# Kernel optimization log

Measured on AMD Instinct MI355X. Metric: run time of the kernel, lower is better.

## Reference

```python
import jax, jax.numpy as jnp
import numpy as np

N, D, H_ENC, NZ, K, H_EXP, C = 32768, 1024, 512, 64, 16, 256, 10


def setup_inputs() -> dict:
    key = jax.random.key(0)
    ks = jax.random.split(key, 12)
    s = 0.02
    return {
        "X": jax.random.normal(ks[0], (N, D), dtype=jnp.float32),
        "enc_W": jax.random.normal(ks[1], (D, H_ENC), dtype=jnp.float32) * s,
        "enc_b": jnp.zeros((H_ENC,), dtype=jnp.float32),
        "z_W": jax.random.normal(ks[2], (H_ENC, NZ), dtype=jnp.float32) * s,
        "z_b": jnp.zeros((NZ,), dtype=jnp.float32),
        "mu": jax.random.normal(ks[3], (K, NZ), dtype=jnp.float32),  # cluster_layer
        "W1": jax.random.normal(ks[4], (K, NZ, H_EXP), dtype=jnp.float32) * s,
        "b1": jnp.zeros((K, H_EXP), dtype=jnp.float32),
        "W2": jax.random.normal(ks[5], (K, H_EXP, C), dtype=jnp.float32) * s,
        "b2": jnp.zeros((K, C), dtype=jnp.float32),
    }


def reference(X, enc_W, enc_b, z_W, z_b, mu, W1, b1, W2, b2):
    # AE encoder: Linear-ReLU -> z_layer
    h = jax.nn.relu(X @ enc_W + enc_b)                 # [N, H_ENC]
    z = h @ z_W + z_b                                  # [N, NZ]
    # source_distribution (Student-t, alpha=1; exponent (alpha+1)/2 = 1)
    dist = jnp.sum((z[:, None, :] - mu[None, :, :]) ** 2, axis=-1)  # [N, K]
    q = 1.0 / (1.0 + dist)
    q = q / jnp.sum(q, axis=1, keepdims=True)          # [N, K]
    # per-expert Linear-ReLU-Linear over full batch (attention=True path)
    eh = jax.nn.relu(jnp.einsum("nd,kdh->nkh", z, W1) + b1[None])  # [N, K, H_EXP]
    logits = jnp.einsum("nkh,khc->nkc", eh, W2) + b2[None]         # [N, K, C]
    # soft combine: preds[:, c] += q[:, k] * logits[:, k, c]
    preds = jnp.einsum("nk,nkc->nc", q, logits)        # [N, C]
    return preds
```

## Files before the change

### kernel.cpp

```cpp
#include <hip/hip_runtime.h>
#include <stdint.h>

#define N_ROWS 32768
#define DIM    1024
#define HENC   512
#define NZ     64
#define KE     16
#define HEXP   256
#define NC     10

typedef __attribute__((ext_vector_type(8))) __bf16 bf16x8;
typedef __attribute__((ext_vector_type(4))) float f32x4;
typedef __attribute__((ext_vector_type(8))) unsigned short u16x8;
typedef __attribute__((ext_vector_type(4))) unsigned short u16x4;

__device__ __forceinline__ unsigned short f2bf(float f) {
    __bf16 h = (__bf16)f;
    return __builtin_bit_cast(unsigned short, h);
}

__device__ __forceinline__ void gload_lds16(void* lds, const void* gsrc) {
    __builtin_amdgcn_global_load_lds(
        (const __attribute__((address_space(1))) unsigned int*)gsrc,
        (__attribute__((address_space(3))) unsigned int*)lds,
        16, 0, 0);
}

#define SWZ(col, row) ((col) ^ (((row) & 7) << 3))

__global__ void prep_weights(const float* __restrict__ enc_W,
                             const float* __restrict__ z_W,
                             const float* __restrict__ W1,
                             const float* __restrict__ W2,
                             unsigned short* __restrict__ enc_Wt,
                             unsigned short* __restrict__ z_Wt,
                             unsigned short* __restrict__ W1t,
                             unsigned short* __restrict__ W2t) {
    const int b = blockIdx.x;
    const int t = threadIdx.x;

    if (b < 200) {
        __shared__ float tile[64][65];
        const float* src;
        unsigned short* dst;
        int R, C, r0, c0;
        if (b < 128) {
            src = enc_W; dst = enc_Wt; R = 1024; C = 512;
            r0 = (b >> 3) * 64; c0 = (b & 7) * 64;
        } else if (b < 136) {
            src = z_W; dst = z_Wt; R = 512; C = 64;
            r0 = (b - 128) * 64; c0 = 0;
        } else {
            int i = b - 136, e = i >> 2, ht = i & 3;
            src = W1 + (size_t)e * (NZ * HEXP);
            dst = W1t + (size_t)e * (HEXP * NZ);
            R = 64; C = 256; r0 = 0; c0 = ht * 64;
        }
        const int rr = t >> 4, cc4 = (t & 15) * 4;
#pragma unroll
        for (int p = 0; p < 4; ++p) {
            float4 v = *(const float4*)(src + (size_t)(r0 + p * 16 + rr) * C + c0 + cc4);
            tile[p * 16 + rr][cc4 + 0] = v.x;
            tile[p * 16 + rr][cc4 + 1] = v.y;
            tile[p * 16 + rr][cc4 + 2] = v.z;
            tile[p * 16 + rr][cc4 + 3] = v.w;
        }
        __syncthreads();
#pragma unroll
        for (int p = 0; p < 4; ++p) {
            const int orow = p * 16 + rr;
            u16x4 o;
            o[0] = f2bf(tile[cc4 + 0][orow]);
            o[1] = f2bf(tile[cc4 + 1][orow]);
            o[2] = f2bf(tile[cc4 + 2][orow]);
            o[3] = f2bf(tile[cc4 + 3][orow]);
            *(u16x4*)(dst + (size_t)(c0 + orow) * R + r0 + cc4) = o;
        }
    } else {
        const int e = b - 200;
        const int h = t;
#pragma unroll
        for (int c = 0; c < 16; ++c) {
            W2t[(size_t)(e * 16 + c) * HEXP + h] =
                (c < NC) ? f2bf(W2[((size_t)e * HEXP + h) * NC + c]) : (unsigned short)0;
        }
    }
}

__launch_bounds__(256, 2)
__global__ void gemm1(const float* __restrict__ X,
                      const unsigned short* __restrict__ Bt,
                      const float* __restrict__ enc_b,
                      const unsigned short* __restrict__ zWt,
                      float* __restrict__ zpart) {
    __shared__ union G1U {
        struct {
            unsigned short As[128][64];
            unsigned short Bs[2][256][64];
        } s;
        unsigned short hbs[128][256];
    } u;
    const int t = threadIdx.x;
    const int lane = t & 63;
    const int w = t >> 6;
    const int g = lane >> 4;
    const int l15 = lane & 15;
    const int l7 = l15 & 7;
    const int wm = (w >> 1) * 64;
    const int wn = (w & 1) * 128;

    const int bid = blockIdx.x;
    const int wgid = (bid & 7) * 64 + (bid >> 3);
    const int m0 = (wgid >> 1) * 128;
    const int n0 = (wgid & 1) * 256;

    const int arow = t >> 4, acolq = t & 15;
    const float* aptr = X + (size_t)(m0 + arow) * DIM + acolq * 4;
    const int ascol = SWZ(acolq * 4, arow);
    const int brow0 = lane >> 3;
    const int bsrccol = SWZ((lane & 7) * 8, brow0);
    const unsigned short* bptr = Bt + (size_t)(n0 + brow0) * DIM + bsrccol;

    f32x4 acc[4][8];
#pragma unroll
    for (int i = 0; i < 4; ++i)
#pragma unroll
        for (int j = 0; j < 8; ++j) acc[i][j] = f32x4{0.f, 0.f, 0.f, 0.f};

    {
#pragma unroll
        for (int it = 0; it < 8; ++it) {
            const int chunk = it * 4 + w;
            gload_lds16(&u.s.Bs[0][chunk * 8][0], bptr + (size_t)chunk * 8 * DIM);
        }
        float4 a[8];
#pragma unroll
        for (int it = 0; it < 8; ++it)
            a[it] = *(const float4*)(aptr + (size_t)it * 16 * DIM);
#pragma unroll
        for (int it = 0; it < 8; ++it) {
            u16x4 p;
            p[0] = f2bf(a[it].x); p[1] = f2bf(a[it].y);
            p[2] = f2bf(a[it].z); p[3] = f2bf(a[it].w);
            *(u16x4*)&u.s.As[it * 16 + arow][ascol] = p;
        }
    }
    __syncthreads();

    float4 an[8];
    for (int step = 0; step < 16; ++step) {
        const int cur = step & 1, nxt = cur ^ 1;

        if (step < 15) {
            const int k1 = (step + 1) * 64;
#pragma unroll
            for (int it = 0; it < 8; ++it) {
                const int chunk = it * 4 + w;
                gload_lds16(&u.s.Bs[nxt][chunk * 8][0],
                            bptr + (size_t)chunk * 8 * DIM + k1);
            }
#pragma unroll
            for (int it = 0; it < 8; ++it)
                an[it] = *(const float4*)(aptr + (size_t)it * 16 * DIM + k1);
        }

#pragma unroll
        for (int kk = 0; kk < 2; ++kk) {
            const int ko = kk * 32 + g * 8;
            const int sko = SWZ(ko, l7);
            bf16x8 af[4], bfr[8];
#pragma unroll
            for (int i = 0; i < 4; ++i)
                af[i] = *(const bf16x8*)&u.s.As[wm + i * 16 + l15][sko];
#pragma unroll
            for (int j = 0; j < 8; ++j)
                bfr[j] = *(const bf16x8*)&u.s.Bs[cur][wn + j * 16 + l15][sko];
#pragma unroll
            for (int i = 0; i < 4; ++i)
#pragma unroll
                for (int j = 0; j < 8; ++j)
                    acc[i][j] = __builtin_amdgcn_mfma_f32_16x16x32_bf16(af[i], bfr[j], acc[i][j], 0, 0, 0);
        }
        __syncthreads();

        if (step < 15) {
#pragma unroll
            for (int it = 0; it < 8; ++it) {
                u16x4 p;
                p[0] = f2bf(an[it].x); p[1] = f2bf(an[it].y);
                p[2] = f2bf(an[it].z); p[3] = f2bf(an[it].w);
                *(u16x4*)&u.s.As[it * 16 + arow][ascol] = p;
            }
        }
        __syncthreads();
    }

#pragma unroll
    for (int j = 0; j < 8; ++j) {
        const int col = wn + j * 16 + l15;
        const float bias = enc_b[n0 + col];
#pragma unroll
        for (int i = 0; i < 4; ++i) {
            const int rb = wm + i * 16 + g * 4;
#pragma unroll
            for (int r = 0; r < 4; ++r) {
                float v = acc[i][j][r] + bias;
                v = v > 0.f ? v : 0.f;
                u.hbs[rb + r][SWZ(col, rb + r)] = f2bf(v);
            }
        }
    }
    __syncthreads();

    {
        f32x4 zacc[2][4];
#pragma unroll
        for (int i2 = 0; i2 < 2; ++i2)
#pragma unroll
            for (int j2 = 0; j2 < 4; ++j2) zacc[i2][j2] = f32x4{0.f, 0.f, 0.f, 0.f};

        const unsigned short* zwB = zWt + n0;
#pragma unroll
        for (int ks = 0; ks < 8; ++ks) {
            const int k = ks * 32 + g * 8;
            bf16x8 bz[4];
#pragma unroll
            for (int j2 = 0; j2 < 4; ++j2)
                bz[j2] = *(const bf16x8*)(zwB + (size_t)(j2 * 16 + l15) * HENC + k);
#pragma unroll
            for (int i2 = 0; i2 < 2; ++i2) {
                const int row = w * 32 + i2 * 16 + l15;
                bf16x8 af = *(const bf16x8*)&u.hbs[row][SWZ(k, row)];
#pragma unroll
                for (int j2 = 0; j2 < 4; ++j2)
                    zacc[i2][j2] = __builtin_amdgcn_mfma_f32_16x16x32_bf16(af, bz[j2], zacc[i2][j2], 0, 0, 0);
            }
        }
        float* zp = zpart + (size_t)(n0 ? 1 : 0) * N_ROWS * NZ;
#pragma unroll
        for (int i2 = 0; i2 < 2; ++i2)
#pragma unroll
            for (int j2 = 0; j2 < 4; ++j2) {
                const int colz = j2 * 16 + l15;
#pragma unroll
                for (int r = 0; r < 4; ++r) {
                    const int rowz = m0 + w * 32 + i2 * 16 + g * 4 + r;
                    zp[(size_t)rowz * NZ + colz] = zacc[i2][j2][r];
                }
            }
    }
}

__launch_bounds__(256, 2)
__global__ void expert_kernel(const float* __restrict__ zpart,
                              const float* __restrict__ z_b,
                              const float* __restrict__ mu,
                              const unsigned short* __restrict__ W1t,
                              const float* __restrict__ b1,
                              const unsigned short* __restrict__ W2t,
                              const float* __restrict__ b2,
                              float* __restrict__ out) {
    __shared__ __align__(16) union SU {
        struct {
            float zs[64][68];
            float mus[16][68];
            float rn[64];
            float mun[16];
        } a;
        struct {
            unsigned short w1s[2][128][64];
            unsigned short ehs[4][16][136];
        } b;
    } su;
    __shared__ float qs[64][16];

    const int t = threadIdx.x;
    const int lane = t & 63;
    const int w = t >> 6;
    const int g = lane >> 4;
    const int l15 = lane & 15;
    const int l7 = l15 & 7;
    const int r0 = blockIdx.x * 64;

    {
        const float* zp0 = zpart;
        const float* zp1 = zpart + (size_t)N_ROWS * NZ;
#pragma unroll
        for (int it = 0; it < 4; ++it) {
            int idx = it * 256 + t;
            int r = idx >> 4, c = (idx & 15) * 4;
            float4 a = *(const float4*)(zp0 + (size_t)(r0 + r) * NZ + c);
            float4 b = *(const float4*)(zp1 + (size_t)(r0 + r) * NZ + c);
            float4 zb = *(const float4*)(z_b + c);
            float4 s;
            s.x = a.x + b.x + zb.x; s.y = a.y + b.y + zb.y;
            s.z = a.z + b.z + zb.z; s.w = a.w + b.w + zb.w;
            *(float4*)&su.a.zs[r][c] = s;
        }
        int r = t >> 4, c = (t & 15) * 4;
        *(float4*)&su.a.mus[r][c] = *(const float4*)(mu + (size_t)r * NZ + c);
    }
    __syncthreads();

    if (t < 64) {
        float s = 0.f;
#pragma unroll
        for (int dq = 0; dq < 16; ++dq) {
            float4 v = *(const float4*)&su.a.zs[t][dq * 4];
            s += v.x * v.x + v.y * v.y + v.z * v.z + v.w * v.w;
        }
        su.a.rn[t] = s;
    } else if (t < 80) {
        int k = t - 64;
        float s = 0.f;
#pragma unroll
        for (int dq = 0; dq < 16; ++dq) {
            float4 v = *(const float4*)&su.a.mus[k][dq * 4];
            s += v.x * v.x + v.y * v.y + v.z * v.z + v.w * v.w;
        }
        su.a.mun[k] = s;
    }
    __syncthreads();

    bf16x8 az[2];
#pragma unroll
    for (int ks = 0; ks < 2; ++ks) {
        int row = w * 16 + l15;
        int ko = ks * 32 + g * 8;
        float4 lo = *(const float4*)&su.a.zs[row][ko];
        float4 hi = *(const float4*)&su.a.zs[row][ko + 4];
        u16x8 tmp;
        tmp[0] = f2bf(lo.x); tmp[1] = f2bf(lo.y); tmp[2] = f2bf(lo.z); tmp[3] = f2bf(lo.w);
        tmp[4] = f2bf(hi.x); tmp[5] = f2bf(hi.y); tmp[6] = f2bf(hi.z); tmp[7] = f2bf(hi.w);
        az[ks] = __builtin_bit_cast(bf16x8, tmp);
    }
    {
        bf16x8 bmu[2];
#pragma unroll
        for (int ks = 0; ks < 2; ++ks) {
            int ko = ks * 32 + g * 8;
            float4 lo = *(const float4*)&su.a.mus[l15][ko];
            float4 hi = *(const float4*)&su.a.mus[l15][ko + 4];
            u16x8 tmp;
            tmp[0] = f2bf(lo.x); tmp[1] = f2bf(lo.y); tmp[2] = f2bf(lo.z); tmp[3] = f2bf(lo.w);
            tmp[4] = f2bf(hi.x); tmp[5] = f2bf(hi.y); tmp[6] = f2bf(hi.z); tmp[7] = f2bf(hi.w);
            bmu[ks] = __builtin_bit_cast(bf16x8, tmp);
        }
        f32x4 dacc = f32x4{0.f, 0.f, 0.f, 0.f};
#pragma unroll
        for (int ks = 0; ks < 2; ++ks)
            dacc = __builtin_amdgcn_mfma_f32_16x16x32_bf16(az[ks], bmu[ks], dacc, 0, 0, 0);
#pragma unroll
        for (int r = 0; r < 4; ++r) {
            int rl = w * 16 + g * 4 + r;
            float dist = su.a.rn[rl] - 2.f * dacc[r] + su.a.mun[l15];
            qs[rl][l15] = 1.f / (1.f + dist);
        }
    }
    __syncthreads();

    if (t < 64) {
        float s = 0.f;
#pragma unroll
        for (int k = 0; k < KE; ++k) s += qs[t][k];
        float inv = 1.f / s;
#pragma unroll
        for (int k = 0; k < KE; ++k) qs[t][k] *= inv;
    }
    __syncthreads();

    const int srow = lane >> 3;
    const int scol = SWZ((lane & 7) * 8, srow);

#pragma unroll
    for (int it = 0; it < 4; ++it) {
        const int chunk = it * 4 + w;
        gload_lds16(&su.b.w1s[0][chunk * 8][0],
                    W1t + (size_t)(chunk * 8 + srow) * NZ + scol);
    }
    __syncthreads();

    float pacc[4] = {0.f, 0.f, 0.f, 0.f};
    unsigned short* eh = &su.b.ehs[w][0][0];

    for (int e = 0; e < KE; ++e) {
        const unsigned short* w2e = W2t + e * (16 * HEXP);
        bf16x8 w2f[8];
#pragma unroll
        for (int hh = 0; hh < 8; ++hh)
            w2f[hh] = *(const bf16x8*)(w2e + (size_t)l15 * HEXP + hh * 32 + g * 8);
        float b1v[2][8];
#pragma unroll
        for (int half = 0; half < 2; ++half)
#pragma unroll
            for (int j = 0; j < 8; ++j)
                b1v[half][j] = b1[e * HEXP + half * 128 + j * 16 + l15];

        f32x4 la = f32x4{0.f, 0.f, 0.f, 0.f};
#pragma unroll
        for (int half = 0; half < 2; ++half) {
            const int i = e * 2 + half;
            const int cur = i & 1, nxt = cur ^ 1;

            if (i + 1 < 2 * KE) {
                const int eg = (i + 1) >> 1;
                const int h1 = ((i + 1) & 1) * 128;
                const unsigned short* src =
                    W1t + (size_t)eg * (HEXP * NZ) + (size_t)(h1 + srow) * NZ + scol;
#pragma unroll
                for (int it = 0; it < 4; ++it) {
                    const int chunk = it * 4 + w;
                    gload_lds16(&su.b.w1s[nxt][chunk * 8][0],
                                src + (size_t)chunk * 8 * NZ);
                }
            }

            f32x4 ea[8];
#pragma unroll
            for (int j = 0; j < 8; ++j) ea[j] = f32x4{0.f, 0.f, 0.f, 0.f};
#pragma unroll
            for (int ks = 0; ks < 2; ++ks) {
                const int sko = SWZ(ks * 32 + g * 8, l7);
#pragma unroll
                for (int j = 0; j < 8; ++j) {
                    bf16x8 bw = *(const bf16x8*)&su.b.w1s[cur][j * 16 + l15][sko];
                    ea[j] = __builtin_amdgcn_mfma_f32_16x16x32_bf16(az[ks], bw, ea[j], 0, 0, 0);
                }
            }
#pragma unroll
            for (int j = 0; j < 8; ++j) {
#pragma unroll
                for (int r = 0; r < 4; ++r) {
                    float v = ea[j][r] + b1v[half][j];
                    v = v > 0.f ? v : 0.f;
                    eh[(g * 4 + r) * 136 + j * 16 + l15] = f2bf(v);
                }
            }
#pragma unroll
            for (int ks2 = 0; ks2 < 4; ++ks2) {
                bf16x8 ef = *(const bf16x8*)&eh[l15 * 136 + ks2 * 32 + g * 8];
                la = __builtin_amdgcn_mfma_f32_16x16x32_bf16(ef, w2f[half * 4 + ks2], la, 0, 0, 0);
            }
            __syncthreads();
        }

        float b2v = (l15 < NC) ? b2[e * NC + l15] : 0.f;
#pragma unroll
        for (int r = 0; r < 4; ++r) {
            int rl = w * 16 + g * 4 + r;
            pacc[r] += qs[rl][e] * (la[r] + b2v);
        }
    }

    if (l15 < NC) {
#pragma unroll
        for (int r = 0; r < 4; ++r) {
            int row = r0 + w * 16 + g * 4 + r;
            out[(size_t)row * NC + l15] = pacc[r];
        }
    }
}

extern "C" void kernel_launch(void* const* d_in, const int* in_sizes, int n_in,
                              void* d_out, int out_size, void* d_ws, size_t ws_size,
                              hipStream_t stream) {
    const float* X     = (const float*)d_in[0];
    const float* enc_W = (const float*)d_in[1];
    const float* enc_b = (const float*)d_in[2];
    const float* z_W   = (const float*)d_in[3];
    const float* z_b   = (const float*)d_in[4];
    const float* mu    = (const float*)d_in[5];
    const float* W1    = (const float*)d_in[6];
    const float* b1    = (const float*)d_in[7];
    const float* W2    = (const float*)d_in[8];
    const float* b2    = (const float*)d_in[9];
    float* out = (float*)d_out;

    char* ws = (char*)d_ws;
    float*          zpart  = (float*)(ws);
    unsigned short* enc_Wt = (unsigned short*)(ws + 16777216);
    unsigned short* z_Wt   = (unsigned short*)(ws + 17825792);
    unsigned short* W1t    = (unsigned short*)(ws + 17891328);
    unsigned short* W2t    = (unsigned short*)(ws + 18415616);

    prep_weights<<<dim3(216), dim3(256), 0, stream>>>(enc_W, z_W, W1, W2,
                                                      enc_Wt, z_Wt, W1t, W2t);
    gemm1<<<dim3(512), dim3(256), 0, stream>>>(X, enc_Wt, enc_b, z_Wt, zpart);
    expert_kernel<<<dim3(512), dim3(256), 0, stream>>>(zpart, z_b, mu, W1t, b1, W2t, b2, out);
}
```

Before: 121.5 us.

## Load B fragments directly from global and double-buffer A in LDS

The B-operand staging through LDS (global_load_lds into a double-buffered Bs) is removed. Each wave now reads its bf16 B fragments straight from global memory into registers every step. The freed LDS holds a double-buffered A tile, which drops one __syncthreads per K-step. In exchange, B reuse across the two M-waves now relies on cache instead of LDS. The global B loads are issued in the same step they are consumed, with no prefetch, so their latency may be exposed.

```diff
diff --git a/kernel.cpp b/kernel.cpp
--- a/kernel.cpp
+++ b/kernel.cpp
@@ -94,10 +94,7 @@
                       const unsigned short* __restrict__ zWt,
                       float* __restrict__ zpart) {
     __shared__ union G1U {
-        struct {
-            unsigned short As[128][64];
-            unsigned short Bs[2][256][64];
-        } s;
+        unsigned short As[2][128][64];
         unsigned short hbs[128][256];
     } u;
     const int t = threadIdx.x;
@@ -117,9 +114,7 @@
     const int arow = t >> 4, acolq = t & 15;
     const float* aptr = X + (size_t)(m0 + arow) * DIM + acolq * 4;
     const int ascol = SWZ(acolq * 4, arow);
-    const int brow0 = lane >> 3;
-    const int bsrccol = SWZ((lane & 7) * 8, brow0);
-    const unsigned short* bptr = Bt + (size_t)(n0 + brow0) * DIM + bsrccol;
+    const unsigned short* bfp = Bt + (size_t)(n0 + wn + l15) * DIM + g * 8;
 
     f32x4 acc[4][8];
 #pragma unroll
@@ -128,11 +123,6 @@
         for (int j = 0; j < 8; ++j) acc[i][j] = f32x4{0.f, 0.f, 0.f, 0.f};
 
     {
-#pragma unroll
-        for (int it = 0; it < 8; ++it) {
-            const int chunk = it * 4 + w;
-            gload_lds16(&u.s.Bs[0][chunk * 8][0], bptr + (size_t)chunk * 8 * DIM);
-        }
         float4 a[8];
 #pragma unroll
         for (int it = 0; it < 8; ++it)
@@ -142,7 +132,7 @@
             u16x4 p;
             p[0] = f2bf(a[it].x); p[1] = f2bf(a[it].y);
             p[2] = f2bf(a[it].z); p[3] = f2bf(a[it].w);
-            *(u16x4*)&u.s.As[it * 16 + arow][ascol] = p;
+            *(u16x4*)&u.As[0][it * 16 + arow][ascol] = p;
         }
     }
     __syncthreads();
@@ -150,15 +140,17 @@
     float4 an[8];
     for (int step = 0; step < 16; ++step) {
         const int cur = step & 1, nxt = cur ^ 1;
+        const int k0 = step * 64;
+
+        bf16x8 bfr[2][8];
+#pragma unroll
+        for (int kk = 0; kk < 2; ++kk)
+#pragma unroll
+            for (int j = 0; j < 8; ++j)
+                bfr[kk][j] = *(const bf16x8*)(bfp + (size_t)(j * 16) * DIM + k0 + kk * 32);
 
         if (step < 15) {
-            const int k1 = (step + 1) * 64;
-#pragma unroll
-            for (int it = 0; it < 8; ++it) {
-                const int chunk = it * 4 + w;
-                gload_lds16(&u.s.Bs[nxt][chunk * 8][0],
-                            bptr + (size_t)chunk * 8 * DIM + k1);
-            }
+            const int k1 = k0 + 64;
 #pragma unroll
             for (int it = 0; it < 8; ++it)
                 an[it] = *(const float4*)(aptr + (size_t)it * 16 * DIM + k1);
@@ -166,22 +158,17 @@
 
 #pragma unroll
         for (int kk = 0; kk < 2; ++kk) {
-            const int ko = kk * 32 + g * 8;
-            const int sko = SWZ(ko, l7);
-            bf16x8 af[4], bfr[8];
+            const int sko = SWZ(kk * 32 + g * 8, l7);
+            bf16x8 af[4];
 #pragma unroll
             for (int i = 0; i < 4; ++i)
-                af[i] = *(const bf16x8*)&u.s.As[wm + i * 16 + l15][sko];
-#pragma unroll
-            for (int j = 0; j < 8; ++j)
-                bfr[j] = *(const bf16x8*)&u.s.Bs[cur][wn + j * 16 + l15][sko];
+                af[i] = *(const bf16x8*)&u.As[cur][wm + i * 16 + l15][sko];
 #pragma unroll
             for (int i = 0; i < 4; ++i)
 #pragma unroll
                 for (int j = 0; j < 8; ++j)
-                    acc[i][j] = __builtin_amdgcn_mfma_f32_16x16x32_bf16(af[i], bfr[j], acc[i][j], 0, 0, 0);
-        }
-        __syncthreads();
+                    acc[i][j] = __builtin_amdgcn_mfma_f32_16x16x32_bf16(af[i], bfr[kk][j], acc[i][j], 0, 0, 0);
+        }
 
         if (step < 15) {
 #pragma unroll
@@ -189,7 +176,7 @@
                 u16x4 p;
                 p[0] = f2bf(an[it].x); p[1] = f2bf(an[it].y);
                 p[2] = f2bf(an[it].z); p[3] = f2bf(an[it].w);
-                *(u16x4*)&u.s.As[it * 16 + arow][ascol] = p;
+                *(u16x4*)&u.As[nxt][it * 16 + arow][ascol] = p;
             }
         }
         __syncthreads();
```

New measurement: 158.1 us. 1.3x slower.

## Software-pipeline expert second-layer MFMA across halves with double-buffered hidden tile

Applied to the files above, without the earlier changes.

Restructures the per-expert loop in the expert kernel so each expert's two 128-wide hidden halves are unrolled explicitly. The second-layer MFMA for half 1 is deferred into the next expert iteration, and a double-buffered per-wave eh tile is used. W1 prefetches into the two LDS slots are reissued at new points. The goal is to overlap LDS round-trips and global loads with MFMA work and cut the serialization around barriers. In exchange, registers stay live longer (w2f, b1v, la) and per-wave LDS use grows, which may hurt occupancy under the 2-block launch bound.

```diff
diff --git a/kernel.cpp b/kernel.cpp
--- a/kernel.cpp
+++ b/kernel.cpp
@@ -269,7 +269,7 @@
         } a;
         struct {
             unsigned short w1s[2][128][64];
-            unsigned short ehs[4][16][136];
+            unsigned short ehs[4][2][16][136];
         } b;
     } su;
     __shared__ float qs[64][16];
@@ -381,40 +381,48 @@
     __syncthreads();
 
     float pacc[4] = {0.f, 0.f, 0.f, 0.f};
-    unsigned short* eh = &su.b.ehs[w][0][0];
+    f32x4 la = f32x4{0.f, 0.f, 0.f, 0.f};
+    bf16x8 w2f[8];
+    float b1v[2][8];
+    unsigned short* eh0 = &su.b.ehs[w][0][0][0];
+    unsigned short* eh1 = &su.b.ehs[w][1][0][0];
 
     for (int e = 0; e < KE; ++e) {
-        const unsigned short* w2e = W2t + e * (16 * HEXP);
-        bf16x8 w2f[8];
-#pragma unroll
-        for (int hh = 0; hh < 8; ++hh)
-            w2f[hh] = *(const bf16x8*)(w2e + (size_t)l15 * HEXP + hh * 32 + g * 8);
-        float b1v[2][8];
-#pragma unroll
-        for (int half = 0; half < 2; ++half)
-#pragma unroll
-            for (int j = 0; j < 8; ++j)
-                b1v[half][j] = b1[e * HEXP + half * 128 + j * 16 + l15];
-
-        f32x4 la = f32x4{0.f, 0.f, 0.f, 0.f};
-#pragma unroll
-        for (int half = 0; half < 2; ++half) {
-            const int i = e * 2 + half;
-            const int cur = i & 1, nxt = cur ^ 1;
-
-            if (i + 1 < 2 * KE) {
-                const int eg = (i + 1) >> 1;
-                const int h1 = ((i + 1) & 1) * 128;
-                const unsigned short* src =
-                    W1t + (size_t)eg * (HEXP * NZ) + (size_t)(h1 + srow) * NZ + scol;
-#pragma unroll
-                for (int it = 0; it < 4; ++it) {
-                    const int chunk = it * 4 + w;
-                    gload_lds16(&su.b.w1s[nxt][chunk * 8][0],
-                                src + (size_t)chunk * 8 * NZ);
-                }
-            }
-
+        if (e > 0) {
+#pragma unroll
+            for (int ks2 = 0; ks2 < 4; ++ks2) {
+                bf16x8 ef = *(const bf16x8*)&eh1[l15 * 136 + ks2 * 32 + g * 8];
+                la = __builtin_amdgcn_mfma_f32_16x16x32_bf16(ef, w2f[4 + ks2], la, 0, 0, 0);
+            }
+            float b2v = (l15 < NC) ? b2[(e - 1) * NC + l15] : 0.f;
+#pragma unroll
+            for (int r = 0; r < 4; ++r) {
+                int rl = w * 16 + g * 4 + r;
+                pacc[r] += qs[rl][e - 1] * (la[r] + b2v);
+            }
+            la = f32x4{0.f, 0.f, 0.f, 0.f};
+        }
+        {
+            const unsigned short* src =
+                W1t + (size_t)e * (HEXP * NZ) + (size_t)(128 + srow) * NZ + scol;
+#pragma unroll
+            for (int it = 0; it < 4; ++it) {
+                const int chunk = it * 4 + w;
+                gload_lds16(&su.b.w1s[1][chunk * 8][0], src + (size_t)chunk * 8 * NZ);
+            }
+        }
+        {
+            const unsigned short* w2e = W2t + e * (16 * HEXP);
+#pragma unroll
+            for (int hh = 0; hh < 8; ++hh)
+                w2f[hh] = *(const bf16x8*)(w2e + (size_t)l15 * HEXP + hh * 32 + g * 8);
+#pragma unroll
+            for (int j = 0; j < 8; ++j) {
+                b1v[0][j] = b1[e * HEXP + j * 16 + l15];
+                b1v[1][j] = b1[e * HEXP + 128 + j * 16 + l15];
+            }
+        }
+        {
             f32x4 ea[8];
 #pragma unroll
             for (int j = 0; j < 8; ++j) ea[j] = f32x4{0.f, 0.f, 0.f, 0.f};
@@ -423,7 +431,7 @@
                 const int sko = SWZ(ks * 32 + g * 8, l7);
 #pragma unroll
                 for (int j = 0; j < 8; ++j) {
-                    bf16x8 bw = *(const bf16x8*)&su.b.w1s[cur][j * 16 + l15][sko];
+                    bf16x8 bw = *(const bf16x8*)&su.b.w1s[0][j * 16 + l15][sko];
                     ea[j] = __builtin_amdgcn_mfma_f32_16x16x32_bf16(az[ks], bw, ea[j], 0, 0, 0);
                 }
             }
@@ -431,24 +439,65 @@
             for (int j = 0; j < 8; ++j) {
 #pragma unroll
                 for (int r = 0; r < 4; ++r) {
-                    float v = ea[j][r] + b1v[half][j];
+                    float v = ea[j][r] + b1v[0][j];
                     v = v > 0.f ? v : 0.f;
-                    eh[(g * 4 + r) * 136 + j * 16 + l15] = f2bf(v);
+                    eh0[(g * 4 + r) * 136 + j * 16 + l15] = f2bf(v);
                 }
             }
-#pragma unroll
-            for (int ks2 = 0; ks2 < 4; ++ks2) {
-                bf16x8 ef = *(const bf16x8*)&eh[l15 * 136 + ks2 * 32 + g * 8];
-                la = __builtin_amdgcn_mfma_f32_16x16x32_bf16(ef, w2f[half * 4 + ks2], la, 0, 0, 0);
-            }
-            __syncthreads();
-        }
-
-        float b2v = (l15 < NC) ? b2[e * NC + l15] : 0.f;
+        }
+        __syncthreads();
+
+#pragma unroll
+        for (int ks2 = 0; ks2 < 4; ++ks2) {
+            bf16x8 ef = *(const bf16x8*)&eh0[l15 * 136 + ks2 * 32 + g * 8];
+            la = __builtin_amdgcn_mfma_f32_16x16x32_bf16(ef, w2f[ks2], la, 0, 0, 0);
+        }
+        if (e + 1 < KE) {
+            const unsigned short* src =
+                W1t + (size_t)(e + 1) * (HEXP * NZ) + (size_t)srow * NZ + scol;
+#pragma unroll
+            for (int it = 0; it < 4; ++it) {
+                const int chunk = it * 4 + w;
+                gload_lds16(&su.b.w1s[0][chunk * 8][0], src + (size_t)chunk * 8 * NZ);
+            }
+        }
+        {
+            f32x4 ea[8];
+#pragma unroll
+            for (int j = 0; j < 8; ++j) ea[j] = f32x4{0.f, 0.f, 0.f, 0.f};
+#pragma unroll
+            for (int ks = 0; ks < 2; ++ks) {
+                const int sko = SWZ(ks * 32 + g * 8, l7);
+#pragma unroll
+                for (int j = 0; j < 8; ++j) {
+                    bf16x8 bw = *(const bf16x8*)&su.b.w1s[1][j * 16 + l15][sko];
+                    ea[j] = __builtin_amdgcn_mfma_f32_16x16x32_bf16(az[ks], bw, ea[j], 0, 0, 0);
+                }
+            }
+#pragma unroll
+            for (int j = 0; j < 8; ++j) {
+#pragma unroll
+                for (int r = 0; r < 4; ++r) {
+                    float v = ea[j][r] + b1v[1][j];
+                    v = v > 0.f ? v : 0.f;
+                    eh1[(g * 4 + r) * 136 + j * 16 + l15] = f2bf(v);
+                }
+            }
+        }
+        __syncthreads();
+    }
+
+    {
+#pragma unroll
+        for (int ks2 = 0; ks2 < 4; ++ks2) {
+            bf16x8 ef = *(const bf16x8*)&eh1[l15 * 136 + ks2 * 32 + g * 8];
+            la = __builtin_amdgcn_mfma_f32_16x16x32_bf16(ef, w2f[4 + ks2], la, 0, 0, 0);
+        }
+        float b2v = (l15 < NC) ? b2[(KE - 1) * NC + l15] : 0.f;
 #pragma unroll
         for (int r = 0; r < 4; ++r) {
             int rl = w * 16 + g * 4 + r;
-            pacc[r] += qs[rl][e] * (la[r] + b2v);
+            pacc[r] += qs[rl][KE - 1] * (la[r] + b2v);
         }
     }
 
```

Result: no change. 120.7 us (median of 10 runs) (-0.7%).
